# Optimization experiments

Hardware: AMD Instinct MI355X
Metric: run time of the kernel (lower is better)

The kernel has to match this reference:

```python
import jax, jax.numpy as jnp
import numpy as np

BSZ, L, H, P = 8, 4096, 512, 256  # batch, seq len, features, complex state dim (conj_sym)
DT_MIN, DT_MAX = 1e-3, 1e-1


def setup_inputs() -> dict:
    key = jax.random.key(0)
    k_u, k_B, k_C, k_D, k_dt = jax.random.split(key, 5)
    u = jax.random.normal(k_u, (BSZ, L, H), dtype=jnp.float32)
    # HiPPO-like stable init for the diagonal state matrix
    Lambda_re = -0.5 * jnp.ones((P,), dtype=jnp.float32)
    Lambda_im = jnp.pi * jnp.arange(P, dtype=jnp.float32)
    # lecun-normal-ish scaling for real/imag parts of B (fan_in = H) and C (fan_in = P)
    B = jax.random.normal(k_B, (P, H, 2), dtype=jnp.float32) / jnp.sqrt(2.0 * H)
    C = jax.random.normal(k_C, (H, P, 2), dtype=jnp.float32) / jnp.sqrt(2.0 * P)
    D = jax.random.normal(k_D, (H,), dtype=jnp.float32)
    log_step = jax.random.uniform(k_dt, (P, 1), dtype=jnp.float32,
                                  minval=jnp.log(DT_MIN), maxval=jnp.log(DT_MAX))
    return {"u": u, "Lambda_re": Lambda_re, "Lambda_im": Lambda_im,
            "B": B, "C": C, "D": D, "log_step": log_step}


def _binop(q_i, q_j):
    """Associative binary operator for diagonal linear recurrence."""
    A_i, b_i = q_i
    A_j, b_j = q_j
    return (A_j * A_i, A_j * b_i + b_j)


def reference(u, Lambda_re, Lambda_im, B, C, D, log_step):
    # --- setup / discretization (zero-order hold) ---
    Lambda = (Lambda_re + 1j * Lambda_im).astype(jnp.complex64)      # (P,)
    B_tilde = (B[..., 0] + 1j * B[..., 1]).astype(jnp.complex64)     # (P,H)
    C_tilde = (C[..., 0] + 1j * C[..., 1]).astype(jnp.complex64)     # (H,P)
    step = jnp.exp(log_step[:, 0])                                   # (P,)
    Lambda_bar = jnp.exp(Lambda * step)                              # (P,)
    B_bar = ((Lambda_bar - 1.0) / Lambda)[:, None] * B_tilde         # (P,H)

    # --- parallel scan over the sequence (diagonal SSM) ---
    Bu = jnp.einsum('blh,ph->blp', u, B_bar)                         # (B,L,P) complex64
    Lam = jnp.broadcast_to(Lambda_bar, Bu.shape)                     # (B,L,P)
    _, xs = jax.lax.associative_scan(_binop, (Lam, Bu), axis=1)      # (B,L,P)

    # --- emissions (factor 2 from conjugate symmetry) + feedthrough ---
    ys = 2.0 * jnp.einsum('blp,hp->blh', xs, C_tilde).real + D * u   # (B,L,H)
    return jax.nn.gelu(ys)
```

## Files before the change

### kernel.cpp

```cpp
#include <hip/hip_runtime.h>
#include <cstdint>
#include <cstddef>

typedef unsigned short u16;
typedef short short8 __attribute__((ext_vector_type(8)));
typedef float floatx4 __attribute__((ext_vector_type(4)));

#define DEVINL __device__ __forceinline__

static constexpr int BSZ = 8, SEQL = 4096, H = 512, P = 256;
static constexpr int M = BSZ * SEQL;
static constexpr int KD = 512;
static constexpr int ND = 512;
static constexpr int CHUNK = 64;
static constexpr int NCH = SEQL / CHUNK;

DEVINL u16 f2bf(float f) {
  union { float f; unsigned u; } v; v.f = f;
  unsigned r = (v.u + 0x7fffu + ((v.u >> 16) & 1u)) >> 16;
  return (u16)r;
}
DEVINL float bf2f(u16 h) {
  union { unsigned u; float f; } v; v.u = ((unsigned)h) << 16; return v.f;
}

DEVINL void gload_lds16(const u16* g, u16* l) {
  __builtin_amdgcn_global_load_lds(
      (const __attribute__((address_space(1))) unsigned*)g,
      (__attribute__((address_space(3))) unsigned*)l, 16, 0, 0);
}

__global__ void setup_kernel(const float* __restrict__ Lre, const float* __restrict__ Lim,
                             const float* __restrict__ logstep,
                             float2* __restrict__ lam, float2* __restrict__ ffac) {
  int p = threadIdx.x;
  if (p >= P) return;
  float lr = Lre[p], li = Lim[p];
  float st = expf(logstep[p]);
  float mag = expf(lr * st);
  float ang = li * st;
  float cr = mag * cosf(ang);
  float ci = mag * sinf(ang);
  lam[p] = make_float2(cr, ci);
  float a = cr - 1.0f, b = ci;
  float den = lr * lr + li * li;
  float fr = (a * lr + b * li) / den;
  float fi = (b * lr - a * li) / den;
  ffac[p] = make_float2(fr, fi);
}

__global__ void bt1_kernel(const float2* __restrict__ Bin,
                           const float2* __restrict__ ffac,
                           u16* __restrict__ bt1) {
  int idx = blockIdx.x * 256 + threadIdx.x;
  int p = idx / H, h = idx % H;
  float2 bv = Bin[(size_t)p * H + h];
  float2 f = ffac[p];
  float br = f.x * bv.x - f.y * bv.y;
  float bi = f.x * bv.y + f.y * bv.x;
  bt1[(size_t)(2 * p) * H + h]     = f2bf(br);
  bt1[(size_t)(2 * p + 1) * H + h] = f2bf(bi);
}

__global__ void bt2_kernel(const float* __restrict__ Cin, u16* __restrict__ bt2) {
  int idx = blockIdx.x * 256 + threadIdx.x;
  float c = Cin[idx];
  float v = (idx & 1) ? -2.0f * c : 2.0f * c;
  bt2[idx] = f2bf(v);
}

__global__ void ucvt_kernel(const float4* __restrict__ uin, ushort4* __restrict__ ubf) {
  int idx = blockIdx.x * 256 + threadIdx.x;
  float4 f = uin[idx];
  ushort4 o;
  o.x = f2bf(f.x); o.y = f2bf(f.y); o.z = f2bf(f.z); o.w = f2bf(f.w);
  ubf[idx] = o;
}

template <int MODE>
__global__ __launch_bounds__(256, 4) void gemm_bt(const u16* __restrict__ A,
                                                  const u16* __restrict__ Bt,
                                                  u16* __restrict__ outBf,
                                                  float* __restrict__ outF,
                                                  const float* __restrict__ Dv,
                                                  const u16* __restrict__ ubf) {
  __shared__ u16 As[128 * 32];
  __shared__ u16 Bs[128 * 32];
  const int tid = threadIdx.x;
  const int bm = blockIdx.x, bn = blockIdx.y;
  const int wave = tid >> 6, lane = tid & 63;
  const int quad = lane >> 4, l16 = lane & 15;
  const int wm = (wave & 1) << 6, wn = (wave >> 1) << 6;

  floatx4 acc[4][4] = {};

  const u16* Ab = A + (size_t)bm * 128 * KD;
  const u16* Bb = Bt + (size_t)bn * 128 * KD;
  const int srow = tid >> 2;
  const int scol = (tid & 3) << 3;

  for (int k0 = 0; k0 < KD; k0 += 32) {
    __syncthreads();
    gload_lds16(Ab + (size_t)srow * KD + k0 + scol,        &As[tid * 8]);
    gload_lds16(Ab + (size_t)(srow + 64) * KD + k0 + scol, &As[2048 + tid * 8]);
    gload_lds16(Bb + (size_t)srow * KD + k0 + scol,        &Bs[tid * 8]);
    gload_lds16(Bb + (size_t)(srow + 64) * KD + k0 + scol, &Bs[2048 + tid * 8]);
    __syncthreads();

    short8 af[4], bf[4];
#pragma unroll
    for (int t = 0; t < 4; t++)
      af[t] = *(const short8*)&As[(wm + t * 16 + l16) * 32 + quad * 8];
#pragma unroll
    for (int t = 0; t < 4; t++)
      bf[t] = *(const short8*)&Bs[(wn + t * 16 + l16) * 32 + quad * 8];
#pragma unroll
    for (int tm = 0; tm < 4; tm++)
#pragma unroll
      for (int tn = 0; tn < 4; tn++)
        acc[tm][tn] = __builtin_amdgcn_mfma_f32_16x16x32_bf16(af[tm], bf[tn], acc[tm][tn], 0, 0, 0);
  }

  const int row_base = bm * 128 + wm + quad * 4;
  const int col_base = bn * 128 + wn + l16;
  float dv[4];
  if (MODE == 1) {
#pragma unroll
    for (int tn = 0; tn < 4; tn++) dv[tn] = Dv[col_base + tn * 16];
  }
#pragma unroll
  for (int tm = 0; tm < 4; tm++) {
#pragma unroll
    for (int tn = 0; tn < 4; tn++) {
      int n = col_base + tn * 16;
#pragma unroll
      for (int r = 0; r < 4; r++) {
        int m = row_base + tm * 16 + r;
        float v = acc[tm][tn][r];
        if (MODE == 0) {
          outBf[(size_t)m * ND + n] = f2bf(v);
        } else {
          float uv = bf2f(ubf[(size_t)m * ND + n]);
          float ys = v + dv[tn] * uv;
          float y3 = ys * ys * ys;
          float t = tanhf(0.7978845608028654f * (ys + 0.044715f * y3));
          outF[(size_t)m * ND + n] = 0.5f * ys * (1.0f + t);
        }
      }
    }
  }
}

__global__ __launch_bounds__(256) void scan_carry(const u16* __restrict__ Bu,
                                                  const float2* __restrict__ lam,
                                                  float2* __restrict__ carry) {
  int p = threadIdx.x;
  int c = blockIdx.x;
  int b = blockIdx.y;
  float2 lm = lam[p];
  float xr = 0.f, xi = 0.f;
  const u16* base = Bu + ((size_t)b * SEQL + (size_t)c * CHUNK) * 512 + 2 * p;
  for (int l = 0; l < CHUNK; l++) {
    unsigned w = *(const unsigned*)(base + (size_t)l * 512);
    float br = bf2f((u16)(w & 0xffffu));
    float bi = bf2f((u16)(w >> 16));
    float nr = lm.x * xr - lm.y * xi + br;
    float ni = lm.x * xi + lm.y * xr + bi;
    xr = nr; xi = ni;
  }
  carry[((size_t)b * NCH + c) * P + p] = make_float2(xr, xi);
}

__global__ __launch_bounds__(256) void scan_prefix(const float2* __restrict__ carry,
                                                   const float2* __restrict__ lam,
                                                   float2* __restrict__ prefix) {
  int p = threadIdx.x;
  int b = blockIdx.x;
  float2 lm = lam[p];
  float ar = lm.x, ai = lm.y;
  for (int i = 0; i < 6; i++) { float nr = ar * ar - ai * ai, ni = 2.f * ar * ai; ar = nr; ai = ni; }
  float pr = 0.f, pi = 0.f;
  for (int c = 0; c < NCH; c++) {
    prefix[((size_t)b * NCH + c) * P + p] = make_float2(pr, pi);
    float2 ca = carry[((size_t)b * NCH + c) * P + p];
    float nr = ar * pr - ai * pi + ca.x;
    float ni = ar * pi + ai * pr + ca.y;
    pr = nr; pi = ni;
  }
}

__global__ __launch_bounds__(256) void scan_apply(u16* __restrict__ Bu,
                                                  const float2* __restrict__ lam,
                                                  const float2* __restrict__ prefix) {
  int p = threadIdx.x;
  int c = blockIdx.x;
  int b = blockIdx.y;
  float2 lm = lam[p];
  float2 pf = prefix[((size_t)b * NCH + c) * P + p];
  float xr = pf.x, xi = pf.y;
  u16* base = Bu + ((size_t)b * SEQL + (size_t)c * CHUNK) * 512 + 2 * p;
  for (int l = 0; l < CHUNK; l++) {
    unsigned* addr = (unsigned*)(base + (size_t)l * 512);
    unsigned w = *addr;
    float br = bf2f((u16)(w & 0xffffu));
    float bi = bf2f((u16)(w >> 16));
    float nr = lm.x * xr - lm.y * xi + br;
    float ni = lm.x * xi + lm.y * xr + bi;
    xr = nr; xi = ni;
    *addr = (unsigned)f2bf(nr) | ((unsigned)f2bf(ni) << 16);
  }
}

extern "C" void kernel_launch(void* const* d_in, const int* in_sizes, int n_in,
                              void* d_out, int out_size, void* d_ws, size_t ws_size,
                              hipStream_t stream) {
  const float* u      = (const float*)d_in[0];
  const float* Lre    = (const float*)d_in[1];
  const float* Lim    = (const float*)d_in[2];
  const float* Bin    = (const float*)d_in[3];
  const float* Cin    = (const float*)d_in[4];
  const float* Dv     = (const float*)d_in[5];
  const float* lstep  = (const float*)d_in[6];
  float* out          = (float*)d_out;

  char* ws = (char*)d_ws;
  float2* lam    = (float2*)(ws + 0);
  float2* ffac   = (float2*)(ws + 2048);
  u16*    bt1    = (u16*)   (ws + 4096);
  u16*    bt2    = (u16*)   (ws + 528384);
  u16*    ubf    = (u16*)   (ws + 1052672);
  u16*    Bu     = (u16*)   (ws + 34607104);
  float2* carry  = (float2*)(ws + 68161536);
  float2* prefix = (float2*)(ws + 69210112);

  setup_kernel<<<1, 256, 0, stream>>>(Lre, Lim, lstep, lam, ffac);
  bt1_kernel<<<(P * H) / 256, 256, 0, stream>>>((const float2*)Bin, ffac, bt1);
  bt2_kernel<<<(H * P * 2) / 256, 256, 0, stream>>>(Cin, bt2);
  ucvt_kernel<<<(M * H / 4) / 256, 256, 0, stream>>>((const float4*)u, (ushort4*)ubf);

  gemm_bt<0><<<dim3(M / 128, ND / 128), 256, 0, stream>>>(ubf, bt1, Bu, nullptr, nullptr, nullptr);

  scan_carry <<<dim3(NCH, BSZ), 256, 0, stream>>>(Bu, lam, carry);
  scan_prefix<<<BSZ, 256, 0, stream>>>(carry, lam, prefix);
  scan_apply <<<dim3(NCH, BSZ), 256, 0, stream>>>(Bu, lam, prefix);

  gemm_bt<1><<<dim3(M / 128, ND / 128), 256, 0, stream>>>(Bu, bt2, nullptr, out, Dv, ubf);
}
```

Measured before the change: 217.2 us.

## Double-buffer GEMM LDS tiles and use exp2/rcp GELU epilogue

The bf16 GEMM's main loop now double-buffers the A and B tiles in LDS and prefetches the next K slice while MFMAs run on the current one. It uses explicit waitcnt, a single barrier per iteration and raised priority around the MFMA block. The GELU epilogue replaces tanhf with the equivalent sigmoid form built from hardware exp2 and reciprocal approximations, which lowers transcendental cost. In exchange, LDS use per block doubles, which may reduce occupancy at 4 blocks per CU, and the fast-math GELU adds a little approximation error.

```diff
diff --git a/kernel.cpp b/kernel.cpp
--- a/kernel.cpp
+++ b/kernel.cpp
@@ -84,8 +84,8 @@
                                                   float* __restrict__ outF,
                                                   const float* __restrict__ Dv,
                                                   const u16* __restrict__ ubf) {
-  __shared__ u16 As[128 * 32];
-  __shared__ u16 Bs[128 * 32];
+  __shared__ u16 As[2][128 * 32];
+  __shared__ u16 Bs[2][128 * 32];
   const int tid = threadIdx.x;
   const int bm = blockIdx.x, bn = blockIdx.y;
   const int wave = tid >> 6, lane = tid & 63;
@@ -99,26 +99,47 @@
   const int srow = tid >> 2;
   const int scol = (tid & 3) << 3;
 
+  gload_lds16(Ab + (size_t)srow * KD + scol,        &As[0][tid * 8]);
+  gload_lds16(Ab + (size_t)(srow + 64) * KD + scol, &As[0][2048 + tid * 8]);
+  gload_lds16(Bb + (size_t)srow * KD + scol,        &Bs[0][tid * 8]);
+  gload_lds16(Bb + (size_t)(srow + 64) * KD + scol, &Bs[0][2048 + tid * 8]);
+  asm volatile("s_waitcnt vmcnt(0)" ::: "memory");
+  __builtin_amdgcn_sched_barrier(0);
+  __builtin_amdgcn_s_barrier();
+
+  int cur = 0;
   for (int k0 = 0; k0 < KD; k0 += 32) {
-    __syncthreads();
-    gload_lds16(Ab + (size_t)srow * KD + k0 + scol,        &As[tid * 8]);
-    gload_lds16(Ab + (size_t)(srow + 64) * KD + k0 + scol, &As[2048 + tid * 8]);
-    gload_lds16(Bb + (size_t)srow * KD + k0 + scol,        &Bs[tid * 8]);
-    gload_lds16(Bb + (size_t)(srow + 64) * KD + k0 + scol, &Bs[2048 + tid * 8]);
-    __syncthreads();
-
-    short8 af[4], bf[4];
+    if (k0 + 32 < KD) {
+      const int nb = cur ^ 1;
+      gload_lds16(Ab + (size_t)srow * KD + (k0 + 32) + scol,        &As[nb][tid * 8]);
+      gload_lds16(Ab + (size_t)(srow + 64) * KD + (k0 + 32) + scol, &As[nb][2048 + tid * 8]);
+      gload_lds16(Bb + (size_t)srow * KD + (k0 + 32) + scol,        &Bs[nb][tid * 8]);
+      gload_lds16(Bb + (size_t)(srow + 64) * KD + (k0 + 32) + scol, &Bs[nb][2048 + tid * 8]);
+    }
+
+    short8 af[4], bfr[4];
 #pragma unroll
     for (int t = 0; t < 4; t++)
-      af[t] = *(const short8*)&As[(wm + t * 16 + l16) * 32 + quad * 8];
+      af[t] = *(const short8*)&As[cur][(wm + t * 16 + l16) * 32 + quad * 8];
 #pragma unroll
     for (int t = 0; t < 4; t++)
-      bf[t] = *(const short8*)&Bs[(wn + t * 16 + l16) * 32 + quad * 8];
+      bfr[t] = *(const short8*)&Bs[cur][(wn + t * 16 + l16) * 32 + quad * 8];
+
+    asm volatile("s_waitcnt lgkmcnt(0)" ::: "memory");
+    __builtin_amdgcn_sched_barrier(0);
+
+    __builtin_amdgcn_s_setprio(1);
 #pragma unroll
     for (int tm = 0; tm < 4; tm++)
 #pragma unroll
       for (int tn = 0; tn < 4; tn++)
-        acc[tm][tn] = __builtin_amdgcn_mfma_f32_16x16x32_bf16(af[tm], bf[tn], acc[tm][tn], 0, 0, 0);
+        acc[tm][tn] = __builtin_amdgcn_mfma_f32_16x16x32_bf16(af[tm], bfr[tn], acc[tm][tn], 0, 0, 0);
+    __builtin_amdgcn_s_setprio(0);
+
+    asm volatile("s_waitcnt vmcnt(0)" ::: "memory");
+    __builtin_amdgcn_sched_barrier(0);
+    __builtin_amdgcn_s_barrier();
+    cur ^= 1;
   }
 
   const int row_base = bm * 128 + wm + quad * 4;
@@ -142,9 +163,9 @@
         } else {
           float uv = bf2f(ubf[(size_t)m * ND + n]);
           float ys = v + dv[tn] * uv;
-          float y3 = ys * ys * ys;
-          float t = tanhf(0.7978845608028654f * (ys + 0.044715f * y3));
-          outF[(size_t)m * ND + n] = 0.5f * ys * (1.0f + t);
+          float zz = ys + 0.044715f * (ys * ys * ys);
+          float e = __builtin_amdgcn_exp2f(-2.3022082f * zz);
+          outF[(size_t)m * ND + n] = ys * __builtin_amdgcn_rcpf(1.0f + e);
         }
       }
     }
```

Measured after the change: 204.0 us. 1.06x faster.
